# Kernel tuning notes

Hardware: AMD Instinct MI355X
Metric: run time of the kernel (lower is better)

## Reference

```python
import jax, jax.numpy as jnp
import numpy as np

INF = 1000000.0
B, S, D, N, H = 2, 2048, 1024, 16, 64
T = 2 * S
NORM = 1.0 / np.sqrt(H)


def _rel_shift(x, k_len, shift=1):
    # x: [b, n, f, t] -> Transformer-XL relative shift -> [b, n, f, k_len]
    b, n, f, t = x.shape
    y = x.reshape(b, n, t, f)[:, :, shift:, :].reshape(b, n, f, t - shift)
    return y[:, :, :, :k_len]


def setup_inputs() -> dict:
    key = jax.random.key(0)
    ks = jax.random.split(key, 16)
    inp = {}
    inp['q'] = jax.random.normal(ks[0], (B, S, D), jnp.float32)
    inp['k'] = jax.random.normal(ks[1], (B, S, D), jnp.float32)
    inp['v'] = jax.random.normal(ks[2], (B, S, D), jnp.float32)
    inp['pos_enc'] = jax.random.normal(ks[3], (T, D), jnp.float32)
    seg_ids = jax.random.randint(ks[4], (B, S), 0, 2)
    inp['seg_mat'] = seg_ids[:, :, None] == seg_ids[:, None, :]  # [B,S,S] bool
    # causal mask: 1 where attention is forbidden (j > i)
    causal = (jnp.arange(S)[None, :] > jnp.arange(S)[:, None]).astype(jnp.float32)
    inp['attn_mask'] = jnp.broadcast_to(causal[None, None], (B, 1, S, S))
    std = np.sqrt(1.0 / (D + N * H))
    inp['qW'] = jax.random.normal(ks[5], (D, N, H), jnp.float32) * std
    inp['kW'] = jax.random.normal(ks[6], (D, N, H), jnp.float32) * std
    inp['kb'] = jnp.zeros((N, H), jnp.float32)
    inp['vW'] = jax.random.normal(ks[7], (D, N, H), jnp.float32) * std
    inp['vb'] = jnp.zeros((N, H), jnp.float32)
    inp['r_w_bias'] = jax.random.uniform(ks[8], (N, H), jnp.float32, 0.0, 0.1)
    inp['r_r_bias'] = jax.random.uniform(ks[9], (N, H), jnp.float32, 0.0, 0.1)
    inp['r_kernel'] = jax.random.uniform(ks[10], (D, N, H), jnp.float32, 0.0, 0.1)
    inp['r_s_bias'] = jax.random.uniform(ks[11], (N, H), jnp.float32, 0.0, 0.1)
    inp['seg_embed'] = jax.random.uniform(ks[12], (2, N, H), jnp.float32, 0.0, 0.1)
    inp['postW'] = jax.random.normal(ks[13], (N, H, D), jnp.float32) * std
    inp['postb'] = jnp.zeros((D,), jnp.float32)
    inp['ln_g'] = jnp.ones((D,), jnp.float32)
    inp['ln_b'] = jnp.zeros((D,), jnp.float32)
    return inp


def reference(q, k, v, pos_enc, seg_mat, attn_mask, qW, kW, kb, vW, vb,
              r_w_bias, r_r_bias, r_kernel, r_s_bias, seg_embed,
              postW, postb, ln_g, ln_b):
    # head projections
    q_head = jnp.einsum('bid,dnh->binh', q, qW) * NORM
    k_head = jnp.einsum('bjd,dnh->bjnh', k, kW) + kb
    v_head = jnp.einsum('bjd,dnh->bjnh', v, vW) + vb
    # content score (r_w_bias also scaled by normalizer)
    content = jnp.einsum('binh,bjnh->bnij', q_head + r_w_bias * NORM, k_head)
    # relative position bias (rel_shift branch, shift=1)
    q_r = q_head + r_r_bias * NORM
    r_head = jnp.einsum('td,dnh->tnh', pos_enc, r_kernel)
    bd = jnp.einsum('bfnh,tnh->bnft', q_r, r_head)  # [B,N,S,T]
    pos_bias = _rel_shift(bd, S, shift=1)           # [B,N,S,S]
    # segment bias
    sb = jnp.einsum('binh,snh->bnis', q_head + r_s_bias * NORM, seg_embed)
    diff, same = sb[..., 0:1], sb[..., 1:2]         # [B,N,S,1]
    seg_bias = jnp.where(seg_mat[:, None], same, diff)  # [B,N,S,S]
    # combine, mask, softmax
    score = content + pos_bias + seg_bias
    score = score.astype(jnp.float32) - INF * attn_mask
    dist = jax.nn.softmax(score, axis=-1)
    # attention output
    attn_vec = jnp.einsum('bnij,bjnh->binh', dist, v_head)
    attn_out = jnp.einsum('binh,nhd->bid', attn_vec, postW) + postb
    # residual + layer norm
    x = q + attn_out
    mu = jnp.mean(x, axis=-1, keepdims=True)
    var = jnp.var(x, axis=-1, keepdims=True)
    return (x - mu) * jax.lax.rsqrt(var + 1e-5) * ln_g + ln_b
```

## Files before the change

### kernel.cpp

```cpp
#include <hip/hip_runtime.h>
#include <hip/hip_bf16.h>

typedef __attribute__((ext_vector_type(8))) short bf16x8;
typedef __attribute__((ext_vector_type(4))) float f32x4;
typedef unsigned short ushort_t;

#define S_LEN 2048
#define DMODEL 1024
#define NORM_F 0.125f

__device__ __forceinline__ short f2b(float x) {
  union { float f; unsigned u; } c; c.f = x;
  unsigned r = (c.u + 0x7FFFu + ((c.u >> 16) & 1u)) >> 16;
  return (short)r;
}
__device__ __forceinline__ float b2f(ushort_t u) {
  union { unsigned u; float f; } c; c.u = ((unsigned)u) << 16; return c.f;
}
__device__ __forceinline__ unsigned cvtpk(float lo, float hi) {
  unsigned r;
  asm volatile("v_cvt_pk_bf16_f32 %0, %1, %2" : "=v"(r) : "v"(lo), "v"(hi));
  return r;
}

__global__ void seg_extract_kernel(const unsigned int* __restrict__ seg_raw,
                                   unsigned* __restrict__ segw) {
  __shared__ int bad_int, bad_flt;
  int tid = threadIdx.x;
  if (tid == 0) { bad_int = 0; bad_flt = 0; }
  __syncthreads();
  for (int i = tid; i < 2048; i += 256) {
    unsigned v = seg_raw[i];
    if (v > 1u) atomicOr(&bad_int, 1);
    if (v != 0u && v != 0x3F800000u) atomicOr(&bad_flt, 1);
  }
  __syncthreads();
  int mode = bad_int ? (bad_flt ? 2 : 1) : 0;
  const unsigned char* u8 = (const unsigned char*)seg_raw;
  int P = blockIdx.x * 256 + tid;
  int b = P >> 11, i = P & 2047;
  size_t off = (size_t)b * S_LEN * S_LEN + i;
  int bit;
  if (mode == 0)      bit = (int)(seg_raw[off] & 1u);
  else if (mode == 1) bit = (seg_raw[off] != 0u) ? 1 : 0;
  else                bit = (int)(u8[off] & 1u);
  unsigned long long mk = __ballot(bit);
  if ((tid & 63) == 0) {
    segw[P >> 5] = (unsigned)mk;
    segw[(P >> 5) + 1] = (unsigned)(mk >> 32);
  }
}

__global__ __launch_bounds__(256) void conv4_kernel(
    const float* __restrict__ s0, const float* __restrict__ s1,
    const float* __restrict__ s2, const float* __restrict__ s3,
    ushort_t* __restrict__ d0, ushort_t* __restrict__ d1,
    ushort_t* __restrict__ d2, ushort_t* __restrict__ d3) {
  int z = blockIdx.y;
  const float* src = z == 0 ? s0 : z == 1 ? s1 : z == 2 ? s2 : s3;
  ushort_t* dst = z == 0 ? d0 : z == 1 ? d1 : z == 2 ? d2 : d3;
  size_t base = ((size_t)blockIdx.x * 256 + threadIdx.x) * 8;
  float4 a = *(const float4*)(src + base);
  float4 b = *(const float4*)(src + base + 4);
  union { ushort_t us[8]; uint4 v; } o;
  o.us[0] = (ushort_t)f2b(a.x); o.us[1] = (ushort_t)f2b(a.y);
  o.us[2] = (ushort_t)f2b(a.z); o.us[3] = (ushort_t)f2b(a.w);
  o.us[4] = (ushort_t)f2b(b.x); o.us[5] = (ushort_t)f2b(b.y);
  o.us[6] = (ushort_t)f2b(b.z); o.us[7] = (ushort_t)f2b(b.w);
  *(uint4*)(dst + base) = o.v;
}

__global__ __launch_bounds__(256) void convT_kernel(
    const float* __restrict__ s0, const float* __restrict__ s1,
    const float* __restrict__ s2, const float* __restrict__ s3,
    const float* __restrict__ s4,
    ushort_t* __restrict__ d0, ushort_t* __restrict__ d1,
    ushort_t* __restrict__ d2, ushort_t* __restrict__ d3,
    ushort_t* __restrict__ d4) {
  int z = blockIdx.z;
  const float* src = z == 0 ? s0 : z == 1 ? s1 : z == 2 ? s2 : z == 3 ? s3 : s4;
  ushort_t* dst = z == 0 ? d0 : z == 1 ? d1 : z == 2 ? d2 : z == 3 ? d3 : d4;
  __shared__ float Tl[64][68];
  int tid = threadIdx.x;
  int k0 = blockIdx.x * 64, n0 = blockIdx.y * 64;
#pragma unroll
  for (int it = 0; it < 4; ++it) {
    int idx = tid + it * 256;
    int r = idx >> 4, c4 = (idx & 15) * 4;
    *(float4*)&Tl[r][c4] = *(const float4*)(src + (size_t)(k0 + r) * 1024 + n0 + c4);
  }
  __syncthreads();
#pragma unroll
  for (int it = 0; it < 2; ++it) {
    int idx = tid + it * 256;
    int nn = idx >> 3, kc = idx & 7;
    union { ushort_t us[8]; uint4 v; } o;
#pragma unroll
    for (int e = 0; e < 8; ++e) o.us[e] = (ushort_t)f2b(Tl[kc * 8 + e][nn]);
    *(uint4*)(dst + (size_t)(n0 + nn) * 1024 + k0 + kc * 8) = o.v;
  }
}

__global__ __launch_bounds__(256) void gemm4_kernel(
    const ushort_t* __restrict__ a0, const ushort_t* __restrict__ a1,
    const ushort_t* __restrict__ a2, const ushort_t* __restrict__ a3,
    const ushort_t* __restrict__ w0, const ushort_t* __restrict__ w1,
    const ushort_t* __restrict__ w2, const ushort_t* __restrict__ w3,
    const float* __restrict__ kb, const float* __restrict__ vb,
    ushort_t* __restrict__ c0, ushort_t* __restrict__ c1,
    ushort_t* __restrict__ c2, ushort_t* __restrict__ c3) {
  const int z = blockIdx.z;
  const ushort_t* A  = z == 0 ? a0 : z == 1 ? a1 : z == 2 ? a2 : a3;
  const ushort_t* Wt = z == 0 ? w0 : z == 1 ? w1 : z == 2 ? w2 : w3;
  const float* bias  = z == 1 ? kb : z == 2 ? vb : (const float*)nullptr;
  ushort_t* C        = z == 0 ? c0 : z == 1 ? c1 : z == 2 ? c2 : c3;
  const float scale  = z == 0 ? NORM_F : 1.0f;

  __shared__ short A_lds[128][40];
  __shared__ short B_lds[128][40];
  const int tid = threadIdx.x;
  const int wave = tid >> 6, lane = tid & 63;
  const int r16 = lane & 15, g = lane >> 4;
  const int wm = wave >> 1, wn = wave & 1;
  const int m0 = blockIdx.x * 128, n0 = blockIdx.y * 128;
  const int sr = tid >> 2, sseg = (tid & 3) * 8;
  f32x4 acc[4][4] = {};
  uint4 ra0 = *(const uint4*)(A + (size_t)(m0 + sr) * 1024 + sseg);
  uint4 ra1 = *(const uint4*)(A + (size_t)(m0 + 64 + sr) * 1024 + sseg);
  uint4 rb0 = *(const uint4*)(Wt + (size_t)(n0 + sr) * 1024 + sseg);
  uint4 rb1 = *(const uint4*)(Wt + (size_t)(n0 + 64 + sr) * 1024 + sseg);
  for (int k0 = 0; k0 < 1024; k0 += 32) {
    *(uint4*)&A_lds[sr][sseg] = ra0;
    *(uint4*)&A_lds[64 + sr][sseg] = ra1;
    *(uint4*)&B_lds[sr][sseg] = rb0;
    *(uint4*)&B_lds[64 + sr][sseg] = rb1;
    __syncthreads();
    if (k0 + 32 < 1024) {
      ra0 = *(const uint4*)(A + (size_t)(m0 + sr) * 1024 + k0 + 32 + sseg);
      ra1 = *(const uint4*)(A + (size_t)(m0 + 64 + sr) * 1024 + k0 + 32 + sseg);
      rb0 = *(const uint4*)(Wt + (size_t)(n0 + sr) * 1024 + k0 + 32 + sseg);
      rb1 = *(const uint4*)(Wt + (size_t)(n0 + 64 + sr) * 1024 + k0 + 32 + sseg);
    }
    bf16x8 af[4], bfr[4];
#pragma unroll
    for (int fm = 0; fm < 4; ++fm)
      af[fm] = *(const bf16x8*)&A_lds[wm * 64 + fm * 16 + r16][g * 8];
#pragma unroll
    for (int fn = 0; fn < 4; ++fn)
      bfr[fn] = *(const bf16x8*)&B_lds[wn * 64 + fn * 16 + r16][g * 8];
#pragma unroll
    for (int fm = 0; fm < 4; ++fm)
#pragma unroll
      for (int fn = 0; fn < 4; ++fn)
        acc[fm][fn] = __builtin_amdgcn_mfma_f32_16x16x32_bf16(af[fm], bfr[fn], acc[fm][fn], 0, 0, 0);
    __syncthreads();
  }
  float bv[4];
#pragma unroll
  for (int fn = 0; fn < 4; ++fn)
    bv[fn] = bias ? bias[n0 + wn * 64 + fn * 16 + r16] : 0.f;
#pragma unroll
  for (int fm = 0; fm < 4; ++fm)
#pragma unroll
    for (int fn = 0; fn < 4; ++fn)
#pragma unroll
      for (int rr = 0; rr < 4; ++rr) {
        float vv = acc[fm][fn][rr] * scale + bv[fn];
        size_t off = (size_t)(m0 + wm * 64 + fm * 16 + g * 4 + rr) * 1024 +
                     n0 + wn * 64 + fn * 16 + r16;
        C[off] = (ushort_t)f2b(vv);
      }
}

__global__ __launch_bounds__(256) void gemm_post_kernel(
    const ushort_t* __restrict__ A, const ushort_t* __restrict__ Wt,
    const float* __restrict__ bias, float* __restrict__ C) {
  __shared__ short A_lds[64][40];
  __shared__ short B_lds[128][40];
  const int tid = threadIdx.x;
  const int wave = tid >> 6, lane = tid & 63;
  const int r16 = lane & 15, g = lane >> 4;
  const int wm = wave >> 1, wn = wave & 1;
  const int m0 = blockIdx.x * 64, n0 = blockIdx.y * 128;
  const int sr = tid >> 2, sseg = (tid & 3) * 8;
  f32x4 acc[2][4] = {};
  uint4 ra0 = *(const uint4*)(A + (size_t)(m0 + sr) * 1024 + sseg);
  uint4 rb0 = *(const uint4*)(Wt + (size_t)(n0 + sr) * 1024 + sseg);
  uint4 rb1 = *(const uint4*)(Wt + (size_t)(n0 + 64 + sr) * 1024 + sseg);
  for (int k0 = 0; k0 < 1024; k0 += 32) {
    *(uint4*)&A_lds[sr][sseg] = ra0;
    *(uint4*)&B_lds[sr][sseg] = rb0;
    *(uint4*)&B_lds[64 + sr][sseg] = rb1;
    __syncthreads();
    if (k0 + 32 < 1024) {
      ra0 = *(const uint4*)(A + (size_t)(m0 + sr) * 1024 + k0 + 32 + sseg);
      rb0 = *(const uint4*)(Wt + (size_t)(n0 + sr) * 1024 + k0 + 32 + sseg);
      rb1 = *(const uint4*)(Wt + (size_t)(n0 + 64 + sr) * 1024 + k0 + 32 + sseg);
    }
    bf16x8 af[2], bfr[4];
#pragma unroll
    for (int fm = 0; fm < 2; ++fm)
      af[fm] = *(const bf16x8*)&A_lds[wm * 32 + fm * 16 + r16][g * 8];
#pragma unroll
    for (int fn = 0; fn < 4; ++fn)
      bfr[fn] = *(const bf16x8*)&B_lds[wn * 64 + fn * 16 + r16][g * 8];
#pragma unroll
    for (int fm = 0; fm < 2; ++fm)
#pragma unroll
      for (int fn = 0; fn < 4; ++fn)
        acc[fm][fn] = __builtin_amdgcn_mfma_f32_16x16x32_bf16(af[fm], bfr[fn], acc[fm][fn], 0, 0, 0);
    __syncthreads();
  }
  float bv[4];
#pragma unroll
  for (int fn = 0; fn < 4; ++fn)
    bv[fn] = bias ? bias[n0 + wn * 64 + fn * 16 + r16] : 0.f;
#pragma unroll
  for (int fm = 0; fm < 2; ++fm)
#pragma unroll
    for (int fn = 0; fn < 4; ++fn)
#pragma unroll
      for (int rr = 0; rr < 4; ++rr) {
        size_t off = (size_t)(m0 + wm * 32 + fm * 16 + g * 4 + rr) * 1024 +
                     n0 + wn * 64 + fn * 16 + r16;
        C[off] = acc[fm][fn][rr] + bv[fn];
      }
}

__global__ __launch_bounds__(64) void qprep_kernel(
    const ushort_t* __restrict__ qh, const float* __restrict__ rwb,
    const float* __restrict__ rrb, const float* __restrict__ rsb,
    const float* __restrict__ sem, ushort_t* __restrict__ qwb,
    ushort_t* __restrict__ qrb, float2* __restrict__ sbp) {
  const int lane = threadIdx.x & 63;
  const int c0 = lane * 16;
  float rwbN[16], rrbN[16], rsbN[16], s0v[16], s1v[16];
#pragma unroll
  for (int u = 0; u < 16; u += 4) {
    *(float4*)&rwbN[u] = *(const float4*)(rwb + c0 + u);
    *(float4*)&rrbN[u] = *(const float4*)(rrb + c0 + u);
    *(float4*)&rsbN[u] = *(const float4*)(rsb + c0 + u);
    *(float4*)&s0v[u]  = *(const float4*)(sem + c0 + u);
    *(float4*)&s1v[u]  = *(const float4*)(sem + 1024 + c0 + u);
  }
#pragma unroll
  for (int u = 0; u < 16; ++u) { rwbN[u] *= NORM_F; rrbN[u] *= NORM_F; rsbN[u] *= NORM_F; }
  for (int r = 0; r < 16; ++r) {
    int row = blockIdx.x * 16 + r;
    const ushort_t* qp = qh + (size_t)row * 1024 + c0;
    union { uint4 v; ushort_t us[8]; } qa, qb;
    qa.v = *(const uint4*)qp; qb.v = *(const uint4*)(qp + 8);
    float p0 = 0.f, p1 = 0.f;
    union { ushort_t us[8]; uint4 v; } w0, w1, r0, r1;
#pragma unroll
    for (int u = 0; u < 16; ++u) {
      float qv = b2f(u < 8 ? qa.us[u] : qb.us[u - 8]);
      ushort_t cw = (ushort_t)f2b(qv + rwbN[u]);
      ushort_t cr = (ushort_t)f2b(qv + rrbN[u]);
      if (u < 8) { w0.us[u] = cw; r0.us[u] = cr; }
      else       { w1.us[u - 8] = cw; r1.us[u - 8] = cr; }
      float qs = qv + rsbN[u];
      p0 += qs * s0v[u]; p1 += qs * s1v[u];
    }
    *(uint4*)(qwb + (size_t)row * 1024 + c0)     = w0.v;
    *(uint4*)(qwb + (size_t)row * 1024 + c0 + 8) = w1.v;
    *(uint4*)(qrb + (size_t)row * 1024 + c0)     = r0.v;
    *(uint4*)(qrb + (size_t)row * 1024 + c0 + 8) = r1.v;
    p0 += __shfl_xor(p0, 1); p0 += __shfl_xor(p0, 2);
    p1 += __shfl_xor(p1, 1); p1 += __shfl_xor(p1, 2);
    if ((lane & 3) == 0) {
      int bI = row >> 11, iI = row & 2047, nI = lane >> 2;
      sbp[((size_t)bI * 16 + nI) * 2048 + iI] = make_float2(p0, p1);
    }
  }
}

__global__ __launch_bounds__(256) void attn_kernel(
    const ushort_t* __restrict__ qwb, const ushort_t* __restrict__ qrb,
    const ushort_t* __restrict__ khb, const ushort_t* __restrict__ vhb,
    const ushort_t* __restrict__ rhb, const float2* __restrict__ sbp,
    const unsigned* __restrict__ segw, ushort_t* __restrict__ opart,
    float* __restrict__ ml) {
  __shared__ short Klds[64][64];
  __shared__ short Rlds[128][64];
  __shared__ short VsT[2][64][72];
  __shared__ short SP[4][1376];

  const int tid = threadIdx.x;
  const int w = tid >> 6, lane = tid & 63;
  const int r16 = lane & 15, g = lane >> 4;
  const int lin = (int)blockIdx.x;
  const int grp = (lin & 7) + ((lin >> 9) << 3);
  const int j = (lin >> 3) & 63;
  const int x = 31 - (j >> 1);
  const int hx = j & 1;
  const int i0 = x * 64;
  const int nh = (x + 2) >> 1;
  const int tbeg = hx ? nh : 0;
  const int tend = hx ? (x + 1) : nh;
  const int n = grp & 15, b = grp >> 4;
  const int BNS = 65536;
  const int rowbase = (b * 16 + n) * 2048 + i0;

  if (tbeg >= tend) {
    const int il0 = w * 16 + g * 4;
#pragma unroll
    for (int rr = 0; rr < 4; ++rr) {
#pragma unroll
      for (int s = 0; s < 4; ++s)
        opart[(size_t)(BNS + rowbase + il0 + rr) * 64 + s * 16 + r16] = 0;
      if (r16 == 0) {
        ml[2 * BNS + rowbase + il0 + rr] = -1e30f;
        ml[3 * BNS + rowbase + il0 + rr] = 0.f;
      }
    }
    return;
  }

  short* SPw = &SP[w][0];
  const int srow = tid >> 3, sg8 = (tid & 7) * 8;

  const int qrow = i0 + w * 16 + r16;
  const ushort_t* qwp = qwb + (size_t)(b * S_LEN + qrow) * DMODEL + n * 64 + g * 8;
  const ushort_t* qrp = qrb + (size_t)(b * S_LEN + qrow) * DMODEL + n * 64 + g * 8;
  bf16x8 qw[2], qr[2];
  qw[0] = *(const bf16x8*)qwp;  qw[1] = *(const bf16x8*)(qwp + 32);
  qr[0] = *(const bf16x8*)qrp;  qr[1] = *(const bf16x8*)(qrp + 32);
  float2 sbv = sbp[((size_t)b * 16 + n) * 2048 + qrow];
  const float sb0 = sbv.x, sb1 = sbv.y;
  const int ai = (segw[b * 64 + (qrow >> 5)] >> (qrow & 31)) & 1;
  const int iw0 = i0 + w * 16;

  {
    const int j0 = tbeg * 64;
    const int W0 = 2048 + j0 - i0 - 63;
#pragma unroll
    for (int it = 0; it < 2; ++it) {
      int qk = tid + it * 256, row = qk >> 3, cl = qk & 7;
      uint4 kv = *(const uint4*)(khb + (size_t)(b * S_LEN + j0 + row) * DMODEL + n * 64 + cl * 8);
      *(uint4*)&Klds[row][(cl ^ (row & 7)) * 8] = kv;
    }
#pragma unroll
    for (int it = 0; it < 4; ++it) {
      int qk = tid + it * 256, row = qk >> 3, cl = qk & 7;
      uint4 rv = *(const uint4*)(rhb + (size_t)(W0 + row) * DMODEL + n * 64 + cl * 8);
      *(uint4*)&Rlds[row][(cl ^ (row & 7)) * 8] = rv;
    }
#pragma unroll
    for (int it = 0; it < 2; ++it) {
      int jj = srow + it * 32;
      union { uint4 v; ushort_t us[8]; } vv;
      vv.v = *(const uint4*)(vhb + (size_t)(b * S_LEN + j0 + jj) * DMODEL + n * 64 + sg8);
#pragma unroll
      for (int e = 0; e < 8; ++e) {
        int hh = sg8 + e;
        VsT[0][hh][((jj >> 3) ^ (hh >> 3)) * 8 + (jj & 7)] = (short)vv.us[e];
      }
    }
  }

  float m_r = -1e30f, l_r = 0.f;
  f32x4 o[4] = {};

  for (int t = tbeg; t < tend; ++t) {
    const int j0 = t * 64;
    const int tt = (t - tbeg) & 1;
    const bool hasn = (t + 1 < tend);
    __syncthreads();

    uint4 kpf[2], rpf[4], vpf[2];
    if (hasn) {
      const int j0n = j0 + 64;
      const int W0n = 2048 + j0n - i0 - 63;
#pragma unroll
      for (int it = 0; it < 2; ++it) {
        int qk = tid + it * 256, row = qk >> 3, cl = qk & 7;
        kpf[it] = *(const uint4*)(khb + (size_t)(b * S_LEN + j0n + row) * DMODEL + n * 64 + cl * 8);
      }
#pragma unroll
      for (int it = 0; it < 4; ++it) {
        int qk = tid + it * 256, row = qk >> 3, cl = qk & 7;
        rpf[it] = *(const uint4*)(rhb + (size_t)(W0n + row) * DMODEL + n * 64 + cl * 8);
      }
#pragma unroll
      for (int it = 0; it < 2; ++it)
        vpf[it] = *(const uint4*)(vhb + (size_t)(b * S_LEN + j0n + srow + it * 32) * DMODEL + n * 64 + sg8);
    }
    unsigned wlo = segw[b * 64 + (j0 >> 5)];
    unsigned whi = segw[b * 64 + (j0 >> 5) + 1];

    __builtin_amdgcn_s_setprio(1);
    f32x4 cf[4] = {};
#pragma unroll
    for (int s = 0; s < 4; ++s) {
      int row = s * 16 + r16;
      bf16x8 k0 = *(const bf16x8*)&Klds[row][(g ^ (row & 7)) * 8];
      bf16x8 k1 = *(const bf16x8*)&Klds[row][((4 + g) ^ (row & 7)) * 8];
      cf[s] = __builtin_amdgcn_mfma_f32_16x16x32_bf16(k0, qw[0], cf[s], 0, 0, 0);
      cf[s] = __builtin_amdgcn_mfma_f32_16x16x32_bf16(k1, qw[1], cf[s], 0, 0, 0);
    }
#pragma unroll
    for (int sp = 0; sp < 5; ++sp) {
      int row = 48 - w * 16 + sp * 16 + r16;
      bf16x8 r0 = *(const bf16x8*)&Rlds[row][(g ^ (row & 7)) * 8];
      bf16x8 r1 = *(const bf16x8*)&Rlds[row][((4 + g) ^ (row & 7)) * 8];
      f32x4 pf = {};
      pf = __builtin_amdgcn_mfma_f32_16x16x32_bf16(r0, qr[0], pf, 0, 0, 0);
      pf = __builtin_amdgcn_mfma_f32_16x16x32_bf16(r1, qr[1], pf, 0, 0, 0);
      uint2 pw;
      pw.x = cvtpk(pf[0], pf[1]);
      pw.y = cvtpk(pf[2], pf[3]);
      *(uint2*)&SPw[r16 * 84 + sp * 16 + g * 4] = pw;
    }
    __builtin_amdgcn_s_setprio(0);
    ushort_t pu[4][4];
#pragma unroll
    for (int s = 0; s < 4; ++s)
#pragma unroll
      for (int rr = 0; rr < 4; ++rr)
        pu[s][rr] = (ushort_t)SPw[r16 * 84 + (15 - r16) + s * 16 + g * 4 + rr];
    float vals[4][4];
    float vmax = -1e30f;
    const bool diag = (t == x);
#pragma unroll
    for (int s = 0; s < 4; ++s) {
      unsigned word = (s < 2) ? wlo : whi;
#pragma unroll
      for (int rr = 0; rr < 4; ++rr) {
        int p = s * 16 + g * 4 + rr;
        int bitv = (word >> (p & 31)) & 1;
        float sv = cf[s][rr] + b2f(pu[s][rr]) + ((bitv == ai) ? sb1 : sb0);
        if (diag && (p > w * 16 + r16)) sv -= 1e6f;
        vals[s][rr] = sv;
        vmax = fmaxf(vmax, sv);
      }
    }
    vmax = fmaxf(vmax, __shfl_xor(vmax, 16));
    vmax = fmaxf(vmax, __shfl_xor(vmax, 32));
    float scl = 1.f;
    bool resc = !__all(vmax <= m_r + 8.f);
    if (resc) {
      float mnew = fmaxf(m_r, vmax);
      scl = __expf(m_r - mnew);
      m_r = mnew;
    }
    float pex[4][4];
    float psum = 0.f;
#pragma unroll
    for (int s = 0; s < 4; ++s)
#pragma unroll
      for (int rr = 0; rr < 4; ++rr) {
        pex[s][rr] = __expf(vals[s][rr] - m_r);
        psum += pex[s][rr];
      }
    l_r = l_r * scl + psum;
#pragma unroll
    for (int s = 0; s < 4; ++s) {
      uint2 pw;
      pw.x = cvtpk(pex[s][0], pex[s][1]);
      pw.y = cvtpk(pex[s][2], pex[s][3]);
      *(uint2*)&SPw[r16 * 72 + s * 16 + g * 4] = pw;
    }
    __syncthreads();

    if (hasn) {
#pragma unroll
      for (int it = 0; it < 2; ++it) {
        int qk = tid + it * 256, row = qk >> 3, cl = qk & 7;
        *(uint4*)&Klds[row][(cl ^ (row & 7)) * 8] = kpf[it];
      }
#pragma unroll
      for (int it = 0; it < 4; ++it) {
        int qk = tid + it * 256, row = qk >> 3, cl = qk & 7;
        *(uint4*)&Rlds[row][(cl ^ (row & 7)) * 8] = rpf[it];
      }
      const int dst = tt ^ 1;
#pragma unroll
      for (int it = 0; it < 2; ++it) {
        int jj = srow + it * 32;
        union { uint4 v; ushort_t us[8]; } vv; vv.v = vpf[it];
#pragma unroll
        for (int e = 0; e < 8; ++e) {
          int hh = sg8 + e;
          VsT[dst][hh][((jj >> 3) ^ (hh >> 3)) * 8 + (jj & 7)] = (short)vv.us[e];
        }
      }
    }
    if (resc) {
      float sclb[4];
#pragma unroll
      for (int rr = 0; rr < 4; ++rr) sclb[rr] = __shfl(scl, g * 4 + rr);
#pragma unroll
      for (int s = 0; s < 4; ++s)
#pragma unroll
        for (int rr = 0; rr < 4; ++rr) o[s][rr] *= sclb[rr];
    }
    bf16x8 pa0 = *(const bf16x8*)&SPw[r16 * 72 + g * 8];
    bf16x8 pa1 = *(const bf16x8*)&SPw[r16 * 72 + 32 + g * 8];
    __builtin_amdgcn_s_setprio(1);
#pragma unroll
    for (int s = 0; s < 4; ++s) {
      int hh = s * 16 + r16;
      bf16x8 v0 = *(const bf16x8*)&VsT[tt][hh][(g ^ (hh >> 3)) * 8];
      bf16x8 v1 = *(const bf16x8*)&VsT[tt][hh][((4 + g) ^ (hh >> 3)) * 8];
      o[s] = __builtin_amdgcn_mfma_f32_16x16x32_bf16(pa0, v0, o[s], 0, 0, 0);
      o[s] = __builtin_amdgcn_mfma_f32_16x16x32_bf16(pa1, v1, o[s], 0, 0, 0);
    }
    __builtin_amdgcn_s_setprio(0);
  }

  float l_row = l_r;
  l_row += __shfl_xor(l_row, 16);
  l_row += __shfl_xor(l_row, 32);
  if (lane < 16) {
    ml[hx * 2 * BNS + rowbase + w * 16 + r16] = m_r;
    ml[(hx * 2 + 1) * BNS + rowbase + w * 16 + r16] = l_row;
  }
#pragma unroll
  for (int s = 0; s < 4; ++s)
#pragma unroll
    for (int rr = 0; rr < 4; ++rr) {
      const int il = w * 16 + g * 4 + rr;
      opart[(size_t)(hx * BNS + rowbase + il) * 64 + s * 16 + r16] = (ushort_t)f2b(o[s][rr]);
    }
}

__global__ __launch_bounds__(256) void merge_kernel(
    const ushort_t* __restrict__ opart, const float* __restrict__ ml,
    ushort_t* __restrict__ av) {
  const int BNS = 65536;
  int row = blockIdx.x * 4 + (threadIdx.x >> 6);
  int lane = threadIdx.x & 63;
  float m0 = ml[row], l0 = ml[BNS + row];
  float m1 = ml[2 * BNS + row], l1 = ml[3 * BNS + row];
  float m = fmaxf(m0, m1);
  float a0 = __expf(m0 - m), a1 = __expf(m1 - m);
  float inv = 1.f / (l0 * a0 + l1 * a1);
  float o0 = b2f(opart[(size_t)row * 64 + lane]);
  float o1 = b2f(opart[(size_t)(BNS + row) * 64 + lane]);
  float ov = (o0 * a0 + o1 * a1) * inv;
  int bI = row >> 15, nI = (row >> 11) & 15, iI = row & 2047;
  av[(size_t)(bI * 2048 + iI) * 1024 + nI * 64 + lane] = (ushort_t)f2b(ov);
}

__global__ __launch_bounds__(256) void ln_kernel(
    const float* __restrict__ q, const float* __restrict__ ao,
    const float* __restrict__ ln_g, const float* __restrict__ ln_b,
    float* __restrict__ out) {
  int row = blockIdx.x;
  const float* xq = q + (size_t)row * 1024;
  const float* xa = ao + (size_t)row * 1024;
  float x[4], lsum = 0.f, lsq = 0.f;
#pragma unroll
  for (int e = 0; e < 4; ++e) {
    int d = threadIdx.x + e * 256;
    x[e] = xq[d] + xa[d];
    lsum += x[e]; lsq += x[e] * x[e];
  }
  for (int off = 1; off < 64; off <<= 1) {
    lsum += __shfl_xor(lsum, off);
    lsq += __shfl_xor(lsq, off);
  }
  __shared__ float red[8];
  int wv = threadIdx.x >> 6, ln = threadIdx.x & 63;
  if (ln == 0) { red[wv] = lsum; red[4 + wv] = lsq; }
  __syncthreads();
  lsum = red[0] + red[1] + red[2] + red[3];
  lsq = red[4] + red[5] + red[6] + red[7];
  float mu = lsum * (1.f / 1024.f);
  float var = lsq * (1.f / 1024.f) - mu * mu;
  float inv = rsqrtf(var + 1e-5f);
#pragma unroll
  for (int e = 0; e < 4; ++e) {
    int d = threadIdx.x + e * 256;
    out[(size_t)row * 1024 + d] = (x[e] - mu) * inv * ln_g[d] + ln_b[d];
  }
}

extern "C" void kernel_launch(void* const* d_in, const int* in_sizes, int n_in,
                              void* d_out, int out_size, void* d_ws, size_t ws_size,
                              hipStream_t stream) {
  const float* q   = (const float*)d_in[0];
  const float* k   = (const float*)d_in[1];
  const float* v   = (const float*)d_in[2];
  const float* pe  = (const float*)d_in[3];
  const void*  seg = d_in[4];
  const float* qW  = (const float*)d_in[6];
  const float* kW  = (const float*)d_in[7];
  const float* kb  = (const float*)d_in[8];
  const float* vW  = (const float*)d_in[9];
  const float* vb  = (const float*)d_in[10];
  const float* rwb = (const float*)d_in[11];
  const float* rrb = (const float*)d_in[12];
  const float* rK  = (const float*)d_in[13];
  const float* rsb = (const float*)d_in[14];
  const float* sem = (const float*)d_in[15];
  const float* pW  = (const float*)d_in[16];
  const float* pb  = (const float*)d_in[17];
  const float* lng = (const float*)d_in[18];
  const float* lnb = (const float*)d_in[19];
  float* out = (float*)d_out;

  const size_t MB = 1u << 20;
  char* W = (char*)d_ws;
  ushort_t* abq  = (ushort_t*)(W + 0 * MB);
  ushort_t* abk  = (ushort_t*)(W + 8 * MB);
  ushort_t* abv  = (ushort_t*)(W + 16 * MB);
  ushort_t* abpe = (ushort_t*)(W + 24 * MB);
  ushort_t* wtq  = (ushort_t*)(W + 32 * MB);
  ushort_t* wtk  = (ushort_t*)(W + 34 * MB);
  ushort_t* wtv  = (ushort_t*)(W + 36 * MB);
  ushort_t* wtr  = (ushort_t*)(W + 38 * MB);
  ushort_t* wtp  = (ushort_t*)(W + 40 * MB);
  ushort_t* qh   = (ushort_t*)(W + 42 * MB);
  ushort_t* kh   = (ushort_t*)(W + 50 * MB);
  ushort_t* vh   = (ushort_t*)(W + 58 * MB);
  ushort_t* rh   = (ushort_t*)(W + 66 * MB);
  unsigned* segw = (unsigned*)(W + 74 * MB);
  float2*   sbp  = (float2*)(W + 74 * MB + 65536);
  float*    ml   = (float*)(W + 75 * MB);
  ushort_t* qwb   = (ushort_t*)(W + 0 * MB);
  ushort_t* qrb   = (ushort_t*)(W + 8 * MB);
  ushort_t* opart = (ushort_t*)(W + 16 * MB);
  ushort_t* av    = (ushort_t*)(W + 42 * MB);
  float*    ao    = (float*)(W + 50 * MB);

  seg_extract_kernel<<<dim3(16), dim3(256), 0, stream>>>((const unsigned int*)seg, segw);
  conv4_kernel<<<dim3(2048, 4), dim3(256), 0, stream>>>(q, k, v, pe, abq, abk, abv, abpe);
  convT_kernel<<<dim3(16, 16, 5), dim3(256), 0, stream>>>(qW, kW, vW, rK, pW,
                                                          wtq, wtk, wtv, wtr, wtp);
  gemm4_kernel<<<dim3(32, 8, 4), dim3(256), 0, stream>>>(
      abq, abk, abv, abpe, wtq, wtk, wtv, wtr, kb, vb, qh, kh, vh, rh);

  qprep_kernel<<<dim3(256), dim3(64), 0, stream>>>(qh, rwb, rrb, rsb, sem, qwb, qrb, sbp);

  attn_kernel<<<dim3(2048), dim3(256), 0, stream>>>(qwb, qrb, kh, vh, rh,
                                                    sbp, segw, opart, ml);
  merge_kernel<<<dim3(16384), dim3(256), 0, stream>>>(opart, ml, av);

  gemm_post_kernel<<<dim3(64, 8), dim3(256), 0, stream>>>(av, wtp, pb, ao);
  ln_kernel<<<dim3(4096), dim3(256), 0, stream>>>(q, ao, lng, lnb, out);
}
```

Before: 274.6 us.

## Fuse fp32-to-bf16 input conversion and q-prep epilogue into projection GEMM

Drops the separate conv4 pass by having the projection GEMM load the fp32 activations directly and pack them to bf16 while staging into LDS. It also folds the qprep kernel into the GEMM epilogue for the q slice, which now writes the bias-shifted q tensors and the segment-bias dot products straight from the accumulators. This removes two kernel launches and the bf16 round trip of the activations and of q_head, at the cost of doubling the global load width for the A operand inside the GEMM loop and adding conversion work there. The segment reduction now uses a 16-lane shuffle across the accumulator layout, and q is no longer rounded to bf16 before the biases are added.

```diff
diff --git a/kernel.cpp b/kernel.cpp
--- a/kernel.cpp
+++ b/kernel.cpp
@@ -21,6 +21,14 @@
   unsigned r;
   asm volatile("v_cvt_pk_bf16_f32 %0, %1, %2" : "=v"(r) : "v"(lo), "v"(hi));
   return r;
+}
+__device__ __forceinline__ uint4 pack8(float4 a, float4 b) {
+  union { ushort_t us[8]; uint4 v; } o;
+  o.us[0] = (ushort_t)f2b(a.x); o.us[1] = (ushort_t)f2b(a.y);
+  o.us[2] = (ushort_t)f2b(a.z); o.us[3] = (ushort_t)f2b(a.w);
+  o.us[4] = (ushort_t)f2b(b.x); o.us[5] = (ushort_t)f2b(b.y);
+  o.us[6] = (ushort_t)f2b(b.z); o.us[7] = (ushort_t)f2b(b.w);
+  return o.v;
 }
 
 __global__ void seg_extract_kernel(const unsigned int* __restrict__ seg_raw,
@@ -51,25 +59,6 @@
   }
 }
 
-__global__ __launch_bounds__(256) void conv4_kernel(
-    const float* __restrict__ s0, const float* __restrict__ s1,
-    const float* __restrict__ s2, const float* __restrict__ s3,
-    ushort_t* __restrict__ d0, ushort_t* __restrict__ d1,
-    ushort_t* __restrict__ d2, ushort_t* __restrict__ d3) {
-  int z = blockIdx.y;
-  const float* src = z == 0 ? s0 : z == 1 ? s1 : z == 2 ? s2 : s3;
-  ushort_t* dst = z == 0 ? d0 : z == 1 ? d1 : z == 2 ? d2 : d3;
-  size_t base = ((size_t)blockIdx.x * 256 + threadIdx.x) * 8;
-  float4 a = *(const float4*)(src + base);
-  float4 b = *(const float4*)(src + base + 4);
-  union { ushort_t us[8]; uint4 v; } o;
-  o.us[0] = (ushort_t)f2b(a.x); o.us[1] = (ushort_t)f2b(a.y);
-  o.us[2] = (ushort_t)f2b(a.z); o.us[3] = (ushort_t)f2b(a.w);
-  o.us[4] = (ushort_t)f2b(b.x); o.us[5] = (ushort_t)f2b(b.y);
-  o.us[6] = (ushort_t)f2b(b.z); o.us[7] = (ushort_t)f2b(b.w);
-  *(uint4*)(dst + base) = o.v;
-}
-
 __global__ __launch_bounds__(256) void convT_kernel(
     const float* __restrict__ s0, const float* __restrict__ s1,
     const float* __restrict__ s2, const float* __restrict__ s3,
@@ -102,19 +91,20 @@
 }
 
 __global__ __launch_bounds__(256) void gemm4_kernel(
-    const ushort_t* __restrict__ a0, const ushort_t* __restrict__ a1,
-    const ushort_t* __restrict__ a2, const ushort_t* __restrict__ a3,
+    const float* __restrict__ a0, const float* __restrict__ a1,
+    const float* __restrict__ a2, const float* __restrict__ a3,
     const ushort_t* __restrict__ w0, const ushort_t* __restrict__ w1,
     const ushort_t* __restrict__ w2, const ushort_t* __restrict__ w3,
     const float* __restrict__ kb, const float* __restrict__ vb,
-    ushort_t* __restrict__ c0, ushort_t* __restrict__ c1,
-    ushort_t* __restrict__ c2, ushort_t* __restrict__ c3) {
+    const float* __restrict__ rwb, const float* __restrict__ rrb,
+    const float* __restrict__ rsb, const float* __restrict__ sem,
+    ushort_t* __restrict__ qwb, ushort_t* __restrict__ qrb,
+    float2* __restrict__ sbp,
+    ushort_t* __restrict__ c1, ushort_t* __restrict__ c2,
+    ushort_t* __restrict__ c3) {
   const int z = blockIdx.z;
-  const ushort_t* A  = z == 0 ? a0 : z == 1 ? a1 : z == 2 ? a2 : a3;
+  const float* A     = z == 0 ? a0 : z == 1 ? a1 : z == 2 ? a2 : a3;
   const ushort_t* Wt = z == 0 ? w0 : z == 1 ? w1 : z == 2 ? w2 : w3;
-  const float* bias  = z == 1 ? kb : z == 2 ? vb : (const float*)nullptr;
-  ushort_t* C        = z == 0 ? c0 : z == 1 ? c1 : z == 2 ? c2 : c3;
-  const float scale  = z == 0 ? NORM_F : 1.0f;
 
   __shared__ short A_lds[128][40];
   __shared__ short B_lds[128][40];
@@ -125,19 +115,23 @@
   const int m0 = blockIdx.x * 128, n0 = blockIdx.y * 128;
   const int sr = tid >> 2, sseg = (tid & 3) * 8;
   f32x4 acc[4][4] = {};
-  uint4 ra0 = *(const uint4*)(A + (size_t)(m0 + sr) * 1024 + sseg);
-  uint4 ra1 = *(const uint4*)(A + (size_t)(m0 + 64 + sr) * 1024 + sseg);
+  float4 fa0a = *(const float4*)(A + (size_t)(m0 + sr) * 1024 + sseg);
+  float4 fa0b = *(const float4*)(A + (size_t)(m0 + sr) * 1024 + sseg + 4);
+  float4 fa1a = *(const float4*)(A + (size_t)(m0 + 64 + sr) * 1024 + sseg);
+  float4 fa1b = *(const float4*)(A + (size_t)(m0 + 64 + sr) * 1024 + sseg + 4);
   uint4 rb0 = *(const uint4*)(Wt + (size_t)(n0 + sr) * 1024 + sseg);
   uint4 rb1 = *(const uint4*)(Wt + (size_t)(n0 + 64 + sr) * 1024 + sseg);
   for (int k0 = 0; k0 < 1024; k0 += 32) {
-    *(uint4*)&A_lds[sr][sseg] = ra0;
-    *(uint4*)&A_lds[64 + sr][sseg] = ra1;
+    *(uint4*)&A_lds[sr][sseg] = pack8(fa0a, fa0b);
+    *(uint4*)&A_lds[64 + sr][sseg] = pack8(fa1a, fa1b);
     *(uint4*)&B_lds[sr][sseg] = rb0;
     *(uint4*)&B_lds[64 + sr][sseg] = rb1;
     __syncthreads();
     if (k0 + 32 < 1024) {
-      ra0 = *(const uint4*)(A + (size_t)(m0 + sr) * 1024 + k0 + 32 + sseg);
-      ra1 = *(const uint4*)(A + (size_t)(m0 + 64 + sr) * 1024 + k0 + 32 + sseg);
+      fa0a = *(const float4*)(A + (size_t)(m0 + sr) * 1024 + k0 + 32 + sseg);
+      fa0b = *(const float4*)(A + (size_t)(m0 + sr) * 1024 + k0 + 32 + sseg + 4);
+      fa1a = *(const float4*)(A + (size_t)(m0 + 64 + sr) * 1024 + k0 + 32 + sseg);
+      fa1b = *(const float4*)(A + (size_t)(m0 + 64 + sr) * 1024 + k0 + 32 + sseg + 4);
       rb0 = *(const uint4*)(Wt + (size_t)(n0 + sr) * 1024 + k0 + 32 + sseg);
       rb1 = *(const uint4*)(Wt + (size_t)(n0 + 64 + sr) * 1024 + k0 + 32 + sseg);
     }
@@ -155,21 +149,63 @@
         acc[fm][fn] = __builtin_amdgcn_mfma_f32_16x16x32_bf16(af[fm], bfr[fn], acc[fm][fn], 0, 0, 0);
     __syncthreads();
   }
-  float bv[4];
-#pragma unroll
-  for (int fn = 0; fn < 4; ++fn)
-    bv[fn] = bias ? bias[n0 + wn * 64 + fn * 16 + r16] : 0.f;
-#pragma unroll
-  for (int fm = 0; fm < 4; ++fm)
+
+  if (z == 0) {
+    float rwbN[4], rrbN[4], rsbN[4], s0c[4], s1c[4];
+#pragma unroll
+    for (int fn = 0; fn < 4; ++fn) {
+      int col = n0 + wn * 64 + fn * 16 + r16;
+      rwbN[fn] = rwb[col] * NORM_F;
+      rrbN[fn] = rrb[col] * NORM_F;
+      rsbN[fn] = rsb[col] * NORM_F;
+      s0c[fn] = sem[col];
+      s1c[fn] = sem[1024 + col];
+    }
+    const int nI = (n0 >> 6) + wn;
+#pragma unroll
+    for (int fm = 0; fm < 4; ++fm)
+#pragma unroll
+      for (int rr = 0; rr < 4; ++rr) {
+        int row = m0 + wm * 64 + fm * 16 + g * 4 + rr;
+        float p0 = 0.f, p1 = 0.f;
+#pragma unroll
+        for (int fn = 0; fn < 4; ++fn) {
+          float vv = acc[fm][fn][rr] * NORM_F;
+          size_t off = (size_t)row * 1024 + n0 + wn * 64 + fn * 16 + r16;
+          qwb[off] = (ushort_t)f2b(vv + rwbN[fn]);
+          qrb[off] = (ushort_t)f2b(vv + rrbN[fn]);
+          float qs = vv + rsbN[fn];
+          p0 += qs * s0c[fn];
+          p1 += qs * s1c[fn];
+        }
+        p0 += __shfl_xor(p0, 1); p0 += __shfl_xor(p0, 2);
+        p0 += __shfl_xor(p0, 4); p0 += __shfl_xor(p0, 8);
+        p1 += __shfl_xor(p1, 1); p1 += __shfl_xor(p1, 2);
+        p1 += __shfl_xor(p1, 4); p1 += __shfl_xor(p1, 8);
+        if (r16 == 0) {
+          int bI = row >> 11, iI = row & 2047;
+          sbp[((size_t)bI * 16 + nI) * 2048 + iI] = make_float2(p0, p1);
+        }
+      }
+  } else {
+    const float* bias = z == 1 ? kb : z == 2 ? vb : (const float*)nullptr;
+    ushort_t* C = z == 1 ? c1 : z == 2 ? c2 : c3;
+    float bv[4];
 #pragma unroll
     for (int fn = 0; fn < 4; ++fn)
-#pragma unroll
-      for (int rr = 0; rr < 4; ++rr) {
-        float vv = acc[fm][fn][rr] * scale + bv[fn];
-        size_t off = (size_t)(m0 + wm * 64 + fm * 16 + g * 4 + rr) * 1024 +
-                     n0 + wn * 64 + fn * 16 + r16;
-        C[off] = (ushort_t)f2b(vv);
-      }
+      bv[fn] = bias ? bias[n0 + wn * 64 + fn * 16 + r16] : 0.f;
+#pragma unroll
+    for (int fm = 0; fm < 4; ++fm)
+#pragma unroll
+      for (int fn = 0; fn < 4; ++fn)
+#pragma unroll
+        for (int rr = 0; rr < 4; ++rr) {
+          float vv = acc[fm][fn][rr] + bv[fn];
+          size_t off = (size_t)(m0 + wm * 64 + fm * 16 + g * 4 + rr) * 1024 +
+                       n0 + wn * 64 + fn * 16 + r16;
+          C[off] = (ushort_t)f2b(vv);
+        }
+  }
 }
 
 __global__ __launch_bounds__(256) void gemm_post_kernel(
@@ -227,54 +263,6 @@
       }
 }
 
-__global__ __launch_bounds__(64) void qprep_kernel(
-    const ushort_t* __restrict__ qh, const float* __restrict__ rwb,
-    const float* __restrict__ rrb, const float* __restrict__ rsb,
-    const float* __restrict__ sem, ushort_t* __restrict__ qwb,
-    ushort_t* __restrict__ qrb, float2* __restrict__ sbp) {
-  const int lane = threadIdx.x & 63;
-  const int c0 = lane * 16;
-  float rwbN[16], rrbN[16], rsbN[16], s0v[16], s1v[16];
-#pragma unroll
-  for (int u = 0; u < 16; u += 4) {
-    *(float4*)&rwbN[u] = *(const float4*)(rwb + c0 + u);
-    *(float4*)&rrbN[u] = *(const float4*)(rrb + c0 + u);
-    *(float4*)&rsbN[u] = *(const float4*)(rsb + c0 + u);
-    *(float4*)&s0v[u]  = *(const float4*)(sem + c0 + u);
-    *(float4*)&s1v[u]  = *(const float4*)(sem + 1024 + c0 + u);
-  }
-#pragma unroll
-  for (int u = 0; u < 16; ++u) { rwbN[u] *= NORM_F; rrbN[u] *= NORM_F; rsbN[u] *= NORM_F; }
-  for (int r = 0; r < 16; ++r) {
-    int row = blockIdx.x * 16 + r;
-    const ushort_t* qp = qh + (size_t)row * 1024 + c0;
-    union { uint4 v; ushort_t us[8]; } qa, qb;
-    qa.v = *(const uint4*)qp; qb.v = *(const uint4*)(qp + 8);
-    float p0 = 0.f, p1 = 0.f;
-    union { ushort_t us[8]; uint4 v; } w0, w1, r0, r1;
-#pragma unroll
-    for (int u = 0; u < 16; ++u) {
-      float qv = b2f(u < 8 ? qa.us[u] : qb.us[u - 8]);
-      ushort_t cw = (ushort_t)f2b(qv + rwbN[u]);
-      ushort_t cr = (ushort_t)f2b(qv + rrbN[u]);
-      if (u < 8) { w0.us[u] = cw; r0.us[u] = cr; }
-      else       { w1.us[u - 8] = cw; r1.us[u - 8] = cr; }
-      float qs = qv + rsbN[u];
-      p0 += qs * s0v[u]; p1 += qs * s1v[u];
-    }
-    *(uint4*)(qwb + (size_t)row * 1024 + c0)     = w0.v;
-    *(uint4*)(qwb + (size_t)row * 1024 + c0 + 8) = w1.v;
-    *(uint4*)(qrb + (size_t)row * 1024 + c0)     = r0.v;
-    *(uint4*)(qrb + (size_t)row * 1024 + c0 + 8) = r1.v;
-    p0 += __shfl_xor(p0, 1); p0 += __shfl_xor(p0, 2);
-    p1 += __shfl_xor(p1, 1); p1 += __shfl_xor(p1, 2);
-    if ((lane & 3) == 0) {
-      int bI = row >> 11, iI = row & 2047, nI = lane >> 2;
-      sbp[((size_t)bI * 16 + nI) * 2048 + iI] = make_float2(p0, p1);
-    }
-  }
-}
-
 __global__ __launch_bounds__(256) void attn_kernel(
     const ushort_t* __restrict__ qwb, const ushort_t* __restrict__ qrb,
     const ushort_t* __restrict__ khb, const ushort_t* __restrict__ vhb,
@@ -603,36 +591,29 @@
 
   const size_t MB = 1u << 20;
   char* W = (char*)d_ws;
-  ushort_t* abq  = (ushort_t*)(W + 0 * MB);
-  ushort_t* abk  = (ushort_t*)(W + 8 * MB);
-  ushort_t* abv  = (ushort_t*)(W + 16 * MB);
-  ushort_t* abpe = (ushort_t*)(W + 24 * MB);
+  ushort_t* qwb  = (ushort_t*)(W + 0 * MB);
+  ushort_t* qrb  = (ushort_t*)(W + 8 * MB);
+  ushort_t* opart = (ushort_t*)(W + 16 * MB);
   ushort_t* wtq  = (ushort_t*)(W + 32 * MB);
   ushort_t* wtk  = (ushort_t*)(W + 34 * MB);
   ushort_t* wtv  = (ushort_t*)(W + 36 * MB);
   ushort_t* wtr  = (ushort_t*)(W + 38 * MB);
   ushort_t* wtp  = (ushort_t*)(W + 40 * MB);
-  ushort_t* qh   = (ushort_t*)(W + 42 * MB);
+  ushort_t* av   = (ushort_t*)(W + 42 * MB);
   ushort_t* kh   = (ushort_t*)(W + 50 * MB);
   ushort_t* vh   = (ushort_t*)(W + 58 * MB);
   ushort_t* rh   = (ushort_t*)(W + 66 * MB);
   unsigned* segw = (unsigned*)(W + 74 * MB);
   float2*   sbp  = (float2*)(W + 74 * MB + 65536);
   float*    ml   = (float*)(W + 75 * MB);
-  ushort_t* qwb   = (ushort_t*)(W + 0 * MB);
-  ushort_t* qrb   = (ushort_t*)(W + 8 * MB);
-  ushort_t* opart = (ushort_t*)(W + 16 * MB);
-  ushort_t* av    = (ushort_t*)(W + 42 * MB);
-  float*    ao    = (float*)(W + 50 * MB);
+  float*    ao   = (float*)(W + 50 * MB);
 
   seg_extract_kernel<<<dim3(16), dim3(256), 0, stream>>>((const unsigned int*)seg, segw);
-  conv4_kernel<<<dim3(2048, 4), dim3(256), 0, stream>>>(q, k, v, pe, abq, abk, abv, abpe);
   convT_kernel<<<dim3(16, 16, 5), dim3(256), 0, stream>>>(qW, kW, vW, rK, pW,
                                                           wtq, wtk, wtv, wtr, wtp);
   gemm4_kernel<<<dim3(32, 8, 4), dim3(256), 0, stream>>>(
-      abq, abk, abv, abpe, wtq, wtk, wtv, wtr, kb, vb, qh, kh, vh, rh);
-
-  qprep_kernel<<<dim3(256), dim3(64), 0, stream>>>(qh, rwb, rrb, rsb, sem, qwb, qrb, sbp);
+      q, k, v, pe, wtq, wtk, wtv, wtr, kb, vb, rwb, rrb, rsb, sem,
+      qwb, qrb, sbp, kh, vh, rh);
 
   attn_kernel<<<dim3(2048), dim3(256), 0, stream>>>(qwb, qrb, kh, vh, rh,
                                                     sbp, segw, opart, ml);
```

Measured after the change: 252.4 us. -8.1%, faster.
